# Kernel optimization log

Hardware: AMD Instinct MI355X
Metric: run time of the kernel (lower is better)

The kernel has to match this reference:

```python
import jax, jax.numpy as jnp
import numpy as np

Q_HEADS, KV_HEADS, DIMS = 16, 4, 1024
HEAD_DIM = DIMS // Q_HEADS          # 64
GROUPS = Q_HEADS // KV_HEADS        # 4
ROPE_BASE = 10000.0


def rope(x):
    # x: (..., s, d) -- standard interleaved rotary embedding, base 10000
    s, d = x.shape[-2], x.shape[-1]
    inv_freq = 1.0 / (ROPE_BASE ** (jnp.arange(0, d, 2, dtype=jnp.float32) / d))
    ang = jnp.arange(s, dtype=jnp.float32)[:, None] * inv_freq[None, :]  # (s, d/2)
    cos, sin = jnp.cos(ang), jnp.sin(ang)
    x1, x2 = x[..., 0::2], x[..., 1::2]
    out = jnp.stack([x1 * cos - x2 * sin, x1 * sin + x2 * cos], axis=-1)
    return out.reshape(x.shape).astype(x.dtype)


def setup_inputs() -> dict:
    key = jax.random.key(0)
    k1, k2, k3, k4, k5, k6 = jax.random.split(key, 6)
    B, S, E = 4, 2048, 1024
    q = jax.random.normal(k1, (B, S, E), dtype=jnp.float32)
    kv = jax.random.normal(k2, (B, S, E), dtype=jnp.float32)
    sc = 1.0 / np.sqrt(E)
    Wq = jax.random.normal(k3, (E, Q_HEADS, HEAD_DIM), dtype=jnp.float32) * sc
    Wk = jax.random.normal(k4, (E, KV_HEADS, HEAD_DIM), dtype=jnp.float32) * sc
    Wv = jax.random.normal(k5, (E, KV_HEADS, HEAD_DIM), dtype=jnp.float32) * sc
    Wo = jax.random.normal(k6, (HEAD_DIM, E), dtype=jnp.float32) / np.sqrt(HEAD_DIM)
    return {"q": q, "kv": kv, "Wq": Wq, "Wk": Wk, "Wv": Wv, "Wo": Wo}


def reference(q, kv, Wq, Wk, Wv, Wo):
    B, S, E = q.shape
    qh = jnp.einsum('bse,ehd->bshd', q, Wq)    # (B,S,Q_HEADS,hd)
    kh = jnp.einsum('bse,ehd->bshd', kv, Wk)   # (B,S,KV_HEADS,hd)
    vh = jnp.einsum('bse,ehd->bshd', kv, Wv)
    # rearrange '... s (h g) d -> ... g h s d' with g=GROUPS (h = KV_HEADS outer)
    qh = qh.reshape(B, S, KV_HEADS, GROUPS, HEAD_DIM).transpose(0, 3, 2, 1, 4)  # (B,g,h,S,d)
    kh = kh.transpose(0, 2, 1, 3)  # (B,h,S,d)
    vh = vh.transpose(0, 2, 1, 3)  # (B,h,S,d)
    qh = rope(qh)
    kh = rope(kh)
    # NOTE: sums over group axis g (faithful to original einsum)
    scores = jnp.einsum('bghsd,bhad->bhsa', qh, kh)
    attn = jax.nn.softmax(scores / (HEAD_DIM ** 0.5), axis=-1)
    out = jnp.einsum('bhsa,bhad->bhsd', attn, vh)  # (B,h,S,d)
    out = out.mean(axis=1)                          # mean over kv heads -> (B,S,d)
    return out @ Wo                                 # (B,S,E)
```

## Files before the change

kernel.cpp:

```cpp
#include <hip/hip_runtime.h>
#include <math.h>

#define SS 2048
#define EE 1024

using bf16x8 = __attribute__((ext_vector_type(8))) short;
using f32x4  = __attribute__((ext_vector_type(4))) float;

__device__ inline short f2bf(float x) {
    unsigned u = __builtin_bit_cast(unsigned, x);
    return (short)((u + 0x7fffu + ((u >> 16) & 1u)) >> 16);
}
__device__ inline short f2bf_r(float x) {
    return (short)((__builtin_bit_cast(unsigned, x) + 0x8000u) >> 16);
}
__device__ inline unsigned pk_bf16(float a, float b) {
    unsigned ua = __builtin_bit_cast(unsigned, a) + 0x8000u;
    unsigned ub = __builtin_bit_cast(unsigned, b) + 0x8000u;
    return __builtin_amdgcn_perm(ub, ua, 0x07060302u);
}
__device__ inline void gl16(const short* g, short* l) {
    __builtin_amdgcn_global_load_lds(
        (const __attribute__((address_space(1))) void*)g,
        (__attribute__((address_space(3))) void*)l, 16, 0, 0);
}

__global__ __launch_bounds__(256) void prep_weights(const float* __restrict__ q,
                                                    const float* __restrict__ kv,
                                                    const float* __restrict__ Wq,
                                                    const float* __restrict__ Wk,
                                                    const float* __restrict__ Wv,
                                                    const float* __restrict__ Wo,
                                                    short* __restrict__ Ab,
                                                    short* __restrict__ Wall,
                                                    short* __restrict__ Wo4,
                                                    float2* __restrict__ RT) {
    if (blockIdx.x < 8192) {
        int gt = blockIdx.x * 256 + threadIdx.x;
        size_t e0 = (size_t)gt * 8;
        const float* src = (e0 < 8388608) ? (q + e0) : (kv + (e0 - 8388608));
        float4 v0 = *(const float4*)src;
        float4 v1 = *(const float4*)(src + 4);
        int4 u;
        u.x = pk_bf16(v0.x, v0.y);
        u.y = pk_bf16(v0.z, v0.w);
        u.z = pk_bf16(v1.x, v1.y);
        u.w = pk_bf16(v1.z, v1.w);
        *(int4*)&Ab[e0] = u;
        return;
    }
    int idx = (blockIdx.x - 8192) * 256 + threadIdx.x;
    int c = idx >> 10, e = idx & 1023;
    int h = c >> 6, d = c & 63;
    const float* p = Wq + (size_t)e * 1024 + h * 256 + d;
    Wall[(size_t)c * 1024 + e] = f2bf(0.18033688011112042f * (p[0] + p[64] + p[128] + p[192]));
    Wall[(size_t)(256 + c) * 1024 + e] = f2bf(Wk[(size_t)e * 256 + c]);
    Wall[(size_t)(512 + c) * 1024 + e] = f2bf(Wv[(size_t)e * 256 + c]);
    Wo4[(size_t)e * 256 + c] = f2bf(0.25f * Wo[(size_t)d * 1024 + e]);
    if (idx < 65536) {
        int s = idx >> 5, ii = idx & 31;
        float freq = __expf(-(float)ii * (9.210340371976184f / 32.0f));
        float sn, cs;
        sincosf((float)s * freq, &sn, &cs);
        RT[idx] = (float2){cs, sn};
    }
}

__global__ __launch_bounds__(256) void proj_kernel(const short* __restrict__ Ab,
                                                   const short* __restrict__ Wall,
                                                   const float2* __restrict__ RT,
                                                   short* __restrict__ Qb,
                                                   short* __restrict__ Kb,
                                                   short* __restrict__ Vt) {
    __shared__ alignas(16) short SMEM[128 * 64 + 64 * 64];
    short (*As)[64] = (short (*)[64])SMEM;
    short (*Bs)[64] = (short (*)[64])(SMEM + 128 * 64);
    int tid = threadIdx.x;
    int wave = tid >> 6, lane = tid & 63, quad = lane >> 4, c16 = lane & 15;
    int wm = wave >> 1, wn = wave & 1;
    int lin = blockIdx.y * 64 + blockIdx.x;
    int X = lin & 7, rr = lin >> 3;
    int m0 = (X * 8 + rr / 12) * 128, n0 = (rr % 12) * 64;
    const short* A = Ab + ((n0 < 256) ? 0 : (size_t)8388608);

    int lr = lane >> 3, lc = lane & 7;
    f32x4 acc[4][2];
    #pragma unroll
    for (int i = 0; i < 4; i++)
        #pragma unroll
        for (int j = 0; j < 2; j++) acc[i][j] = (f32x4){0.f, 0.f, 0.f, 0.f};

    for (int k0 = 0; k0 < 1024; k0 += 64) {
        __syncthreads();
        #pragma unroll
        for (int i = 0; i < 4; i++) {
            int seg = wave * 4 + i;
            int r = seg * 8 + lr;
            gl16(&A[(size_t)(m0 + r) * 1024 + k0 + lc * 8], &As[seg * 8][0]);
        }
        #pragma unroll
        for (int i = 0; i < 2; i++) {
            int seg = wave * 2 + i;
            int r = seg * 8 + lr;
            gl16(&Wall[(size_t)(n0 + r) * 1024 + k0 + lc * 8], &Bs[seg * 8][0]);
        }
        __syncthreads();
        #pragma unroll
        for (int ks = 0; ks < 64; ks += 32) {
            bf16x8 af[4], bfr[2];
            #pragma unroll
            for (int mt = 0; mt < 4; mt++)
                af[mt] = *(const bf16x8*)&As[wm * 64 + mt * 16 + c16][ks + quad * 8];
            #pragma unroll
            for (int nt = 0; nt < 2; nt++)
                bfr[nt] = *(const bf16x8*)&Bs[wn * 32 + nt * 16 + c16][ks + quad * 8];
            #pragma unroll
            for (int mt = 0; mt < 4; mt++)
                #pragma unroll
                for (int nt = 0; nt < 2; nt++)
                    acc[mt][nt] = __builtin_amdgcn_mfma_f32_16x16x32_bf16(
                        af[mt], bfr[nt], acc[mt][nt], 0, 0, 0);
        }
    }
    __syncthreads();
    if (n0 < 512) {
        #pragma unroll
        for (int mt = 0; mt < 4; mt++) {
            #pragma unroll
            for (int nt = 0; nt < 2; nt++) {
                int cl = wn * 32 + nt * 16 + c16;
                int ii = cl >> 1;
                float sgn = (lane & 1) ? 1.0f : -1.0f;
                f32x4 v = acc[mt][nt];
                #pragma unroll
                for (int r = 0; r < 4; r++) {
                    int rl = wm * 64 + mt * 16 + quad * 4 + r;
                    float2 cs = RT[((m0 + rl) & (SS - 1)) * 32 + ii];
                    float other = __shfl_xor(v[r], 1);
                    As[rl][cl] = f2bf_r(v[r] * cs.x + sgn * cs.y * other);
                }
            }
        }
        __syncthreads();
        short* dstb = (n0 < 256) ? Qb : Kb;
        int nc0 = n0 & 255;
        #pragma unroll
        for (int i = 0; i < 4; i++) {
            int id = i * 256 + tid, r = id >> 3, ch = id & 7;
            *(int4*)&dstb[(size_t)(m0 + r) * 256 + nc0 + ch * 8] =
                *(const int4*)&As[r][ch * 8];
        }
    } else {
        short (*Lt)[136] = (short(*)[136])SMEM;
        #pragma unroll
        for (int mt = 0; mt < 4; mt++) {
            #pragma unroll
            for (int nt = 0; nt < 2; nt++) {
                int cl = wn * 32 + nt * 16 + c16;
                int sl = wm * 64 + mt * 16 + quad * 4;
                f32x4 v = acc[mt][nt];
                uint2 u;
                u.x = pk_bf16(v[0], v[1]);
                u.y = pk_bf16(v[2], v[3]);
                *(uint2*)&Lt[cl][sl] = u;
            }
        }
        __syncthreads();
        int b = m0 >> 11, s0 = m0 & (SS - 1), c0 = n0 - 512;
        #pragma unroll
        for (int i = 0; i < 4; i++) {
            int id = i * 256 + tid, c = id >> 4, ch = id & 15;
            *(int4*)&Vt[((size_t)(b * 256 + c0 + c)) * SS + s0 + ch * 8] =
                *(const int4*)&Lt[c][ch * 8];
        }
    }
}

__global__ __launch_bounds__(512, 4) void attn_kernel(const short* __restrict__ Qb,
                                                      const short* __restrict__ Kb,
                                                      const short* __restrict__ Vt,
                                                      short* __restrict__ Ob) {
    __shared__ alignas(16) short SM[40960];
    short (*Ks)[2][64][64] = (short (*)[2][64][64])(SM + 8192);
    short (*Vs)[2][64][64] = (short (*)[2][64][64])(SM + 24576);
    int tid = threadIdx.x;
    int wave = tid >> 6, lane = tid & 63, quad = lane >> 4, c16 = lane & 15;
    int rq = wave & 3, kh = wave >> 2;
    int lin = blockIdx.y * 32 + blockIdx.x;
    int X = lin & 7, rr = lin >> 3;
    int bh = X * 2 + (rr >> 5), qt = rr & 31;
    int q0 = qt * 64;
    size_t qkbase = (size_t)(bh >> 2) * SS * 256 + (bh & 3) * 64;
    size_t vtbase = (size_t)(bh * 64) * SS;

    const short* qrow = Qb + qkbase + (size_t)(q0 + rq * 16 + c16) * 256 + quad * 8;
    bf16x8 aq0 = *(const bf16x8*)qrow;
    bf16x8 aq1 = *(const bf16x8*)(qrow + 32);

    short (*Ps)[64] = (short (*)[64])(SM + wave * 1024);

    int swz = (c16 & 7) << 3;

    float lsum[4] = {0.f, 0.f, 0.f, 0.f};
    f32x4 o[4];
    #pragma unroll
    for (int dt = 0; dt < 4; dt++) o[dt] = (f32x4){0.f, 0.f, 0.f, 0.f};

    int sr = tid >> 3, sch = tid & 7;
    int wsz = (sch * 8) ^ ((sr & 7) << 3);
    const short* kbase = Kb + qkbase;
    const short* vbase = Vt + vtbase + (size_t)sr * SS;

    int4 kr0 = *(const int4*)&kbase[(size_t)sr * 256 + sch * 8];
    int4 kr1 = *(const int4*)&kbase[(size_t)(1024 + sr) * 256 + sch * 8];
    int4 vr0 = *(const int4*)&vbase[sch * 8];
    int4 vr1 = *(const int4*)&vbase[1024 + sch * 8];
    *(int4*)&Ks[0][0][sr][wsz] = kr0;
    *(int4*)&Ks[0][1][sr][wsz] = kr1;
    *(int4*)&Vs[0][0][sr][wsz] = vr0;
    *(int4*)&Vs[0][1][sr][wsz] = vr1;
    kr0 = *(const int4*)&kbase[(size_t)(64 + sr) * 256 + sch * 8];
    kr1 = *(const int4*)&kbase[(size_t)(1024 + 64 + sr) * 256 + sch * 8];
    vr0 = *(const int4*)&vbase[64 + sch * 8];
    vr1 = *(const int4*)&vbase[1024 + 64 + sch * 8];
    __syncthreads();

    #pragma unroll 1
    for (int kt = 0; kt < 16; kt++) {
        int p = kt & 1;
        if (kt < 15) {
            *(int4*)&Ks[p ^ 1][0][sr][wsz] = kr0;
            *(int4*)&Ks[p ^ 1][1][sr][wsz] = kr1;
            *(int4*)&Vs[p ^ 1][0][sr][wsz] = vr0;
            *(int4*)&Vs[p ^ 1][1][sr][wsz] = vr1;
        }
        if (kt < 14) {
            int a1 = (kt + 2) * 64;
            kr0 = *(const int4*)&kbase[(size_t)(a1 + sr) * 256 + sch * 8];
            kr1 = *(const int4*)&kbase[(size_t)(1024 + a1 + sr) * 256 + sch * 8];
            vr0 = *(const int4*)&vbase[a1 + sch * 8];
            vr1 = *(const int4*)&vbase[1024 + a1 + sch * 8];
        }
        f32x4 sv[4];
        #pragma unroll
        for (int nt = 0; nt < 4; nt++) sv[nt] = (f32x4){0.f, 0.f, 0.f, 0.f};
        __builtin_amdgcn_s_setprio(1);
        #pragma unroll
        for (int nt = 0; nt < 4; nt++) {
            bf16x8 bk0 = *(const bf16x8*)&Ks[p][kh][nt * 16 + c16][(quad * 8) ^ swz];
            bf16x8 bk1 = *(const bf16x8*)&Ks[p][kh][nt * 16 + c16][(32 + quad * 8) ^ swz];
            sv[nt] = __builtin_amdgcn_mfma_f32_16x16x32_bf16(aq0, bk0, sv[nt], 0, 0, 0);
            sv[nt] = __builtin_amdgcn_mfma_f32_16x16x32_bf16(aq1, bk1, sv[nt], 0, 0, 0);
        }
        __builtin_amdgcn_s_setprio(0);
        #pragma unroll
        for (int nt = 0; nt < 4; nt++)
            #pragma unroll
            for (int r = 0; r < 4; r++) sv[nt][r] = __builtin_exp2f(sv[nt][r]);
        #pragma unroll
        for (int r = 0; r < 4; r++)
            lsum[r] += (sv[0][r] + sv[1][r]) + (sv[2][r] + sv[3][r]);
        #pragma unroll
        for (int nt = 0; nt < 4; nt++)
            #pragma unroll
            for (int r = 0; r < 4; r++) {
                int lrow = quad * 4 + r;
                Ps[lrow][(nt * 16 + c16) ^ ((lrow & 7) << 3)] = f2bf_r(sv[nt][r]);
            }
        #pragma unroll
        for (int ks = 0; ks < 64; ks += 32) {
            bf16x8 ap = *(const bf16x8*)&Ps[c16][(ks + quad * 8) ^ swz];
            __builtin_amdgcn_s_setprio(1);
            #pragma unroll
            for (int dt = 0; dt < 4; dt++) {
                bf16x8 bv = *(const bf16x8*)&Vs[p][kh][dt * 16 + c16][(ks + quad * 8) ^ swz];
                o[dt] = __builtin_amdgcn_mfma_f32_16x16x32_bf16(ap, bv, o[dt], 0, 0, 0);
            }
            __builtin_amdgcn_s_setprio(0);
        }
        __syncthreads();
    }
    #pragma unroll
    for (int off = 1; off < 16; off <<= 1)
        #pragma unroll
        for (int r = 0; r < 4; r++) lsum[r] += __shfl_xor(lsum[r], off);

    float (*Ox)[68] = (float (*)[68])SM;
    float* Lx = (float*)(SM + 9216);
    short (*Ot)[72] = (short (*)[72])(SM + 12288);
    int base = rq * 16 + quad * 4;
    if (wave >= 4) {
        #pragma unroll
        for (int dt = 0; dt < 4; dt++)
            #pragma unroll
            for (int r = 0; r < 4; r++)
                Ox[base + r][dt * 16 + c16] = o[dt][r];
        if (c16 == 0)
            #pragma unroll
            for (int r = 0; r < 4; r++) Lx[base + r] = lsum[r];
    }
    __syncthreads();
    if (wave < 4) {
        #pragma unroll
        for (int r = 0; r < 4; r++) {
            float rl = __builtin_amdgcn_rcpf(lsum[r] + Lx[base + r]);
            #pragma unroll
            for (int dt = 0; dt < 4; dt++)
                Ot[base + r][dt * 16 + c16] =
                    f2bf_r((o[dt][r] + Ox[base + r][dt * 16 + c16]) * rl);
        }
    }
    __syncthreads();
    {
        int r = tid >> 3, ch = tid & 7;
        int b = bh >> 2, h = bh & 3;
        *(int4*)&Ob[((size_t)(b * SS + q0 + r)) * 256 + h * 64 + ch * 8] =
            *(const int4*)&Ot[r][ch * 8];
    }
}

__global__ __launch_bounds__(256) void outproj_kernel(const short* __restrict__ Ob,
                                                      const short* __restrict__ Wo4,
                                                      float* __restrict__ out) {
    __shared__ alignas(16) short As[128][72];
    __shared__ alignas(16) short Bs[64][72];
    int tid = threadIdx.x;
    int wave = tid >> 6, lane = tid & 63, quad = lane >> 4, c16 = lane & 15;
    int lin = blockIdx.y * 64 + blockIdx.x;
    int X = lin & 7, rr = lin >> 3;
    int m0 = (X * 8 + (rr >> 4)) * 128, n0 = (rr & 15) * 64;

    f32x4 acc[2][4];
    #pragma unroll
    for (int i = 0; i < 2; i++)
        #pragma unroll
        for (int j = 0; j < 4; j++) acc[i][j] = (f32x4){0.f, 0.f, 0.f, 0.f};

    for (int k0 = 0; k0 < 256; k0 += 64) {
        #pragma unroll
        for (int i = 0; i < 4; i++) {
            int id = i * 256 + tid, r = id >> 3, ch = id & 7;
            *(int4*)&As[r][ch * 8] =
                *(const int4*)&Ob[(size_t)(m0 + r) * 256 + k0 + ch * 8];
        }
        #pragma unroll
        for (int i = 0; i < 2; i++) {
            int id = i * 256 + tid, r = id >> 3, ch = id & 7;
            *(int4*)&Bs[r][ch * 8] =
                *(const int4*)&Wo4[(size_t)(n0 + r) * 256 + k0 + ch * 8];
        }
        __syncthreads();
        #pragma unroll
        for (int ks = 0; ks < 64; ks += 32) {
            bf16x8 af[2], bfr[4];
            #pragma unroll
            for (int mt = 0; mt < 2; mt++)
                af[mt] = *(const bf16x8*)&As[wave * 32 + mt * 16 + c16][ks + quad * 8];
            #pragma unroll
            for (int nt = 0; nt < 4; nt++)
                bfr[nt] = *(const bf16x8*)&Bs[nt * 16 + c16][ks + quad * 8];
            #pragma unroll
            for (int mt = 0; mt < 2; mt++)
                #pragma unroll
                for (int nt = 0; nt < 4; nt++)
                    acc[mt][nt] = __builtin_amdgcn_mfma_f32_16x16x32_bf16(
                        af[mt], bfr[nt], acc[mt][nt], 0, 0, 0);
        }
        __syncthreads();
    }
    #pragma unroll
    for (int mt = 0; mt < 2; mt++)
        #pragma unroll
        for (int nt = 0; nt < 4; nt++) {
            int col = n0 + nt * 16 + c16;
            int rowb = m0 + wave * 32 + mt * 16 + quad * 4;
            #pragma unroll
            for (int r = 0; r < 4; r++)
                out[(size_t)(rowb + r) * 1024 + col] = acc[mt][nt][r];
        }
}

extern "C" void kernel_launch(void* const* d_in, const int* in_sizes, int n_in,
                              void* d_out, int out_size, void* d_ws, size_t ws_size,
                              hipStream_t stream) {
    const float* q  = (const float*)d_in[0];
    const float* kv = (const float*)d_in[1];
    const float* Wq = (const float*)d_in[2];
    const float* Wk = (const float*)d_in[3];
    const float* Wv = (const float*)d_in[4];
    const float* Wo = (const float*)d_in[5];
    float* out = (float*)d_out;

    short* Qb    = (short*)d_ws;
    short* Kb    = Qb + 2097152;
    short* Vt    = Kb + 2097152;
    short* Wall  = Vt + 2097152;
    short* Wo4   = Wall + 786432;
    float2* RT   = (float2*)(Wo4 + 262144);
    short* Ob    = (short*)(RT + 65536);
    short* Ab    = Ob + 2097152;

    prep_weights<<<9216, 256, 0, stream>>>(q, kv, Wq, Wk, Wv, Wo, Ab, Wall, Wo4, RT);

    proj_kernel<<<dim3(64, 12), 256, 0, stream>>>(Ab, Wall, RT, Qb, Kb, Vt);

    attn_kernel<<<dim3(32, 16), 512, 0, stream>>>(Qb, Kb, Vt, Ob);

    outproj_kernel<<<dim3(64, 16), 256, 0, stream>>>(Ob, Wo4, out);
}
```

Measured before the change: 192.5 us.

## Drop intra-block KV split in attention; use 4-wave blocks iterating full sequence

The attention kernel no longer splits the key/value sequence between two halves of an 8-wave block. Each 4-wave block now loops over all 32 key tiles itself, which removes the cross-wave merge of partial outputs and row sums through shared memory and one barrier. Shared memory per block is halved, so more blocks can be resident per CU. The cost is a serial loop twice as long per block and half as many waves per block to hide latency.

```diff
diff --git a/kernel.cpp b/kernel.cpp
--- a/kernel.cpp
+++ b/kernel.cpp
@@ -176,16 +176,16 @@
     }
 }
 
-__global__ __launch_bounds__(512, 4) void attn_kernel(const short* __restrict__ Qb,
+__global__ __launch_bounds__(256, 4) void attn_kernel(const short* __restrict__ Qb,
                                                       const short* __restrict__ Kb,
                                                       const short* __restrict__ Vt,
                                                       short* __restrict__ Ob) {
-    __shared__ alignas(16) short SM[40960];
-    short (*Ks)[2][64][64] = (short (*)[2][64][64])(SM + 8192);
-    short (*Vs)[2][64][64] = (short (*)[2][64][64])(SM + 24576);
+    __shared__ alignas(16) short SM[20480];
+    short (*Ks)[64][64] = (short (*)[64][64])(SM + 4096);
+    short (*Vs)[64][64] = (short (*)[64][64])(SM + 12288);
     int tid = threadIdx.x;
     int wave = tid >> 6, lane = tid & 63, quad = lane >> 4, c16 = lane & 15;
-    int rq = wave & 3, kh = wave >> 2;
+    int rq = wave;
     int lin = blockIdx.y * 32 + blockIdx.x;
     int X = lin & 7, rr = lin >> 3;
     int bh = X * 2 + (rr >> 5), qt = rr & 31;
@@ -198,7 +198,6 @@
     bf16x8 aq1 = *(const bf16x8*)(qrow + 32);
 
     short (*Ps)[64] = (short (*)[64])(SM + wave * 1024);
-
     int swz = (c16 & 7) << 3;
 
     float lsum[4] = {0.f, 0.f, 0.f, 0.f};
@@ -207,39 +206,39 @@
     for (int dt = 0; dt < 4; dt++) o[dt] = (f32x4){0.f, 0.f, 0.f, 0.f};
 
     int sr = tid >> 3, sch = tid & 7;
-    int wsz = (sch * 8) ^ ((sr & 7) << 3);
+    int wc = (sch * 8) ^ ((sr & 7) << 3);
     const short* kbase = Kb + qkbase;
-    const short* vbase = Vt + vtbase + (size_t)sr * SS;
-
-    int4 kr0 = *(const int4*)&kbase[(size_t)sr * 256 + sch * 8];
-    int4 kr1 = *(const int4*)&kbase[(size_t)(1024 + sr) * 256 + sch * 8];
-    int4 vr0 = *(const int4*)&vbase[sch * 8];
-    int4 vr1 = *(const int4*)&vbase[1024 + sch * 8];
-    *(int4*)&Ks[0][0][sr][wsz] = kr0;
-    *(int4*)&Ks[0][1][sr][wsz] = kr1;
-    *(int4*)&Vs[0][0][sr][wsz] = vr0;
-    *(int4*)&Vs[0][1][sr][wsz] = vr1;
-    kr0 = *(const int4*)&kbase[(size_t)(64 + sr) * 256 + sch * 8];
-    kr1 = *(const int4*)&kbase[(size_t)(1024 + 64 + sr) * 256 + sch * 8];
-    vr0 = *(const int4*)&vbase[64 + sch * 8];
-    vr1 = *(const int4*)&vbase[1024 + 64 + sch * 8];
+    const short* vbase = Vt + vtbase;
+
+    int4 kra = *(const int4*)&kbase[(size_t)sr * 256 + sch * 8];
+    int4 krb = *(const int4*)&kbase[(size_t)(sr + 32) * 256 + sch * 8];
+    int4 vra = *(const int4*)&vbase[(size_t)sr * SS + sch * 8];
+    int4 vrb = *(const int4*)&vbase[(size_t)(sr + 32) * SS + sch * 8];
+    *(int4*)&Ks[0][sr][wc] = kra;
+    *(int4*)&Ks[0][sr + 32][wc] = krb;
+    *(int4*)&Vs[0][sr][wc] = vra;
+    *(int4*)&Vs[0][sr + 32][wc] = vrb;
+    kra = *(const int4*)&kbase[(size_t)(64 + sr) * 256 + sch * 8];
+    krb = *(const int4*)&kbase[(size_t)(64 + sr + 32) * 256 + sch * 8];
+    vra = *(const int4*)&vbase[(size_t)sr * SS + 64 + sch * 8];
+    vrb = *(const int4*)&vbase[(size_t)(sr + 32) * SS + 64 + sch * 8];
     __syncthreads();
 
     #pragma unroll 1
-    for (int kt = 0; kt < 16; kt++) {
+    for (int kt = 0; kt < 32; kt++) {
         int p = kt & 1;
-        if (kt < 15) {
-            *(int4*)&Ks[p ^ 1][0][sr][wsz] = kr0;
-            *(int4*)&Ks[p ^ 1][1][sr][wsz] = kr1;
-            *(int4*)&Vs[p ^ 1][0][sr][wsz] = vr0;
-            *(int4*)&Vs[p ^ 1][1][sr][wsz] = vr1;
-        }
-        if (kt < 14) {
-            int a1 = (kt + 2) * 64;
-            kr0 = *(const int4*)&kbase[(size_t)(a1 + sr) * 256 + sch * 8];
-            kr1 = *(const int4*)&kbase[(size_t)(1024 + a1 + sr) * 256 + sch * 8];
-            vr0 = *(const int4*)&vbase[a1 + sch * 8];
-            vr1 = *(const int4*)&vbase[1024 + a1 + sch * 8];
+        if (kt < 31) {
+            *(int4*)&Ks[p ^ 1][sr][wc] = kra;
+            *(int4*)&Ks[p ^ 1][sr + 32][wc] = krb;
+            *(int4*)&Vs[p ^ 1][sr][wc] = vra;
+            *(int4*)&Vs[p ^ 1][sr + 32][wc] = vrb;
+        }
+        if (kt < 30) {
+            int a2 = (kt + 2) * 64;
+            kra = *(const int4*)&kbase[(size_t)(a2 + sr) * 256 + sch * 8];
+            krb = *(const int4*)&kbase[(size_t)(a2 + sr + 32) * 256 + sch * 8];
+            vra = *(const int4*)&vbase[(size_t)sr * SS + a2 + sch * 8];
+            vrb = *(const int4*)&vbase[(size_t)(sr + 32) * SS + a2 + sch * 8];
         }
         f32x4 sv[4];
         #pragma unroll
@@ -247,8 +246,8 @@
         __builtin_amdgcn_s_setprio(1);
         #pragma unroll
         for (int nt = 0; nt < 4; nt++) {
-            bf16x8 bk0 = *(const bf16x8*)&Ks[p][kh][nt * 16 + c16][(quad * 8) ^ swz];
-            bf16x8 bk1 = *(const bf16x8*)&Ks[p][kh][nt * 16 + c16][(32 + quad * 8) ^ swz];
+            bf16x8 bk0 = *(const bf16x8*)&Ks[p][nt * 16 + c16][(quad * 8) ^ swz];
+            bf16x8 bk1 = *(const bf16x8*)&Ks[p][nt * 16 + c16][(32 + quad * 8) ^ swz];
             sv[nt] = __builtin_amdgcn_mfma_f32_16x16x32_bf16(aq0, bk0, sv[nt], 0, 0, 0);
             sv[nt] = __builtin_amdgcn_mfma_f32_16x16x32_bf16(aq1, bk1, sv[nt], 0, 0, 0);
         }
@@ -273,7 +272,7 @@
             __builtin_amdgcn_s_setprio(1);
             #pragma unroll
             for (int dt = 0; dt < 4; dt++) {
-                bf16x8 bv = *(const bf16x8*)&Vs[p][kh][dt * 16 + c16][(ks + quad * 8) ^ swz];
+                bf16x8 bv = *(const bf16x8*)&Vs[p][dt * 16 + c16][(ks + quad * 8) ^ swz];
                 o[dt] = __builtin_amdgcn_mfma_f32_16x16x32_bf16(ap, bv, o[dt], 0, 0, 0);
             }
             __builtin_amdgcn_s_setprio(0);
@@ -285,37 +284,24 @@
         #pragma unroll
         for (int r = 0; r < 4; r++) lsum[r] += __shfl_xor(lsum[r], off);
 
-    float (*Ox)[68] = (float (*)[68])SM;
-    float* Lx = (float*)(SM + 9216);
-    short (*Ot)[72] = (short (*)[72])(SM + 12288);
+    short (*Ot)[72] = (short (*)[72])(SM + 4096);
     int base = rq * 16 + quad * 4;
-    if (wave >= 4) {
+    #pragma unroll
+    for (int r = 0; r < 4; r++) {
+        float rl = __builtin_amdgcn_rcpf(lsum[r]);
         #pragma unroll
         for (int dt = 0; dt < 4; dt++)
-            #pragma unroll
-            for (int r = 0; r < 4; r++)
-                Ox[base + r][dt * 16 + c16] = o[dt][r];
-        if (c16 == 0)
-            #pragma unroll
-            for (int r = 0; r < 4; r++) Lx[base + r] = lsum[r];
-    }
-    __syncthreads();
-    if (wave < 4) {
-        #pragma unroll
-        for (int r = 0; r < 4; r++) {
-            float rl = __builtin_amdgcn_rcpf(lsum[r] + Lx[base + r]);
-            #pragma unroll
-            for (int dt = 0; dt < 4; dt++)
-                Ot[base + r][dt * 16 + c16] =
-                    f2bf_r((o[dt][r] + Ox[base + r][dt * 16 + c16]) * rl);
-        }
+            Ot[base + r][dt * 16 + c16] = f2bf_r(o[dt][r] * rl);
     }
     __syncthreads();
     {
-        int r = tid >> 3, ch = tid & 7;
         int b = bh >> 2, h = bh & 3;
-        *(int4*)&Ob[((size_t)(b * SS + q0 + r)) * 256 + h * 64 + ch * 8] =
-            *(const int4*)&Ot[r][ch * 8];
+        #pragma unroll
+        for (int i = 0; i < 2; i++) {
+            int id = i * 256 + tid, r = id >> 3, ch = id & 7;
+            *(int4*)&Ob[((size_t)(b * SS + q0 + r)) * 256 + h * 64 + ch * 8] =
+                *(const int4*)&Ot[r][ch * 8];
+        }
     }
 }
 
@@ -404,7 +390,7 @@
 
     proj_kernel<<<dim3(64, 12), 256, 0, stream>>>(Ab, Wall, RT, Qb, Kb, Vt);
 
-    attn_kernel<<<dim3(32, 16), 512, 0, stream>>>(Qb, Kb, Vt, Ob);
+    attn_kernel<<<dim3(32, 16), 256, 0, stream>>>(Qb, Kb, Vt, Ob);
 
     outproj_kernel<<<dim3(64, 16), 256, 0, stream>>>(Ob, Wo4, out);
 }
```

Measured after the change: 196.9 us. 2.3% more time.
